# Kernel optimization log

Measured on AMD Instinct MI355X. Metric: run time of the kernel, lower is better.

Reference implementation:

```python
import jax, jax.numpy as jnp
import numpy as np

FP8_MAX = 448.0   # torch.finfo(float8_e4m3fn).max
BLK = 128         # block_size = [128, 128] for weights; [1, 128] for activations
E, H, I, T, TOPK = 8, 2048, 1408, 512, 2
FP8 = jnp.float8_e4m3fn


def fp8_round(x):
    """Round-trip through float8_e4m3fn (simulates .to(float8_e4m3fn))."""
    return jnp.clip(x, -FP8_MAX, FP8_MAX).astype(FP8).astype(jnp.float32)


def setup_inputs() -> dict:
    key = jax.random.key(0)
    ks = jax.random.split(key, 7)
    hidden_states = jax.random.normal(ks[0], (T, H), jnp.float32)
    top_k_index = jax.random.randint(ks[1], (T, TOPK), 0, E)
    top_k_weights = jax.random.uniform(ks[2], (T, TOPK), jnp.float32)
    # FP8 weight codes (stored as fp32 values exactly representable in e4m3fn)
    gate_up_proj = fp8_round(jax.random.normal(ks[3], (E, 2 * I, H), jnp.float32))
    gate_up_proj_scale_inv = jax.random.uniform(ks[4], (E, (2 * I) // BLK, H // BLK), jnp.float32, 1e-4, 1e-2)
    down_proj = fp8_round(jax.random.normal(ks[5], (E, H, I), jnp.float32))
    down_proj_scale_inv = jax.random.uniform(ks[6], (E, H // BLK, I // BLK), jnp.float32, 1e-4, 1e-2)
    return {
        "hidden_states": hidden_states,
        "top_k_index": top_k_index,
        "top_k_weights": top_k_weights,
        "gate_up_proj": gate_up_proj,
        "gate_up_proj_scale_inv": gate_up_proj_scale_inv,
        "down_proj": down_proj,
        "down_proj_scale_inv": down_proj_scale_inv,
    }


def dequant_weight(wq, s):
    # wq: [E, N, K] fp8 codes; s: [E, N//BLK, K//BLK] per-128x128-block scale_inv
    e, n, k = wq.shape
    wb = wq.reshape(e, n // BLK, BLK, k // BLK, BLK)
    return (wb * s[:, :, None, :, None]).reshape(e, n, k)


def quant_dequant_act(x):
    # dynamic per-(row, 128-block) fp8 activation quantization, then dequant
    shp = x.shape
    xb = x.reshape(shp[:-1] + (shp[-1] // BLK, BLK))
    amax = jnp.max(jnp.abs(xb), axis=-1, keepdims=True)
    scale = jnp.maximum(amax, 1e-12) / FP8_MAX
    q = fp8_round(xb / scale)
    return (q * scale).reshape(shp)


def reference(hidden_states, top_k_index, top_k_weights, gate_up_proj,
              gate_up_proj_scale_inv, down_proj, down_proj_scale_inv):
    w_gu = dequant_weight(gate_up_proj, gate_up_proj_scale_inv)  # [E, 2I, H]
    w_d = dequant_weight(down_proj, down_proj_scale_inv)         # [E, H, I]
    # activation quantization is per-token-block, so unrouted tokens are
    # unaffected; dense per-expert compute + combine-weight mask equals the
    # original gather/scatter loop exactly (unrouted contributions weight 0).
    x = quant_dequant_act(hidden_states)                         # [T, H]
    gate_up = jnp.einsum('th,enh->etn', x, w_gu)                 # [E, T, 2I]
    gate, up = jnp.split(gate_up, 2, axis=-1)
    h = jax.nn.silu(gate) * up                                   # [E, T, I]
    h = quant_dequant_act(h)
    down = jnp.einsum('eti,ehi->eth', h, w_d)                    # [E, T, H]
    # combine[t, e] = sum over top-k slots routing token t to expert e
    combine = jnp.sum(jax.nn.one_hot(top_k_index, E, dtype=top_k_weights.dtype)
                      * top_k_weights[..., None], axis=1)        # [T, E]
    out = jnp.einsum('eth,te->th', down, combine)
    return out.astype(hidden_states.dtype)
```

## Files before the change

kernel.cpp:

```cpp
#include <hip/hip_runtime.h>
#include <math.h>

#define NE 8
#define HD 2048
#define ID 1408
#define NT 512
#define FP8MAX 448.0f

typedef __attribute__((ext_vector_type(4))) float floatx4;

__device__ __forceinline__ floatx4 fzero4() {
    floatx4 z; z.x = 0.f; z.y = 0.f; z.z = 0.f; z.w = 0.f; return z;
}

#define OFF_OFFS  0
#define OFF_TOK   1024
#define OFF_WGT   8192
#define OFF_ENT   16384
#define OFF_XSG   32768
#define OFF_XG    131072
#define OFF_HS    (3*1024*1024)
#define OFF_HQ    (3*1024*1024 + 65536)
#define OFF_GU0   (5*1024*1024)
#define OFF_GU1   (17*1024*1024)

#define LDA 136

__global__ void route_kernel(const int* __restrict__ tki,
                             const float* __restrict__ tkw,
                             int* __restrict__ offs,
                             int* __restrict__ tok,
                             float* __restrict__ wgt,
                             int* __restrict__ ent) {
    __shared__ int cnt[NE];
    __shared__ int cur[NE];
    __shared__ int base[NE + 1];
    int tid = threadIdx.x;
    if (tid < NE) { cnt[tid] = 0; cur[tid] = 0; }
    __syncthreads();
    int e = tki[tid];
    atomicAdd(&cnt[e], 1);
    __syncthreads();
    if (tid == 0) {
        int s = 0;
        for (int i = 0; i < NE; i++) { base[i] = s; s += cnt[i]; }
        base[NE] = s;
    }
    __syncthreads();
    int pos = atomicAdd(&cur[e], 1);
    int j = base[e] + pos;
    tok[j] = tid >> 1;
    wgt[j] = tkw[tid];
    ent[tid] = j;
    if (tid <= NE) offs[tid] = base[tid];
}

__global__ void quant_x_kernel(const float* __restrict__ x,
                               const int* __restrict__ ent,
                               unsigned char* __restrict__ xg,
                               float* __restrict__ xsg) {
    int wid = (blockIdx.x * 256 + threadIdx.x) >> 6;
    int lane = threadIdx.x & 63;
    int t = wid >> 4;
    int b = wid & 15;
    const float2 v = *(const float2*)(x + (long)t * HD + b * 128 + lane * 2);
    float am = fmaxf(fabsf(v.x), fabsf(v.y));
    #pragma unroll
    for (int m = 32; m; m >>= 1) am = fmaxf(am, __shfl_xor(am, m));
    float scale = fmaxf(am, 1e-12f) / FP8MAX;
    int p = __builtin_amdgcn_cvt_pk_fp8_f32(v.x / scale, v.y / scale, 0, false);
    unsigned short pk = (unsigned short)(p & 0xffff);
    int e0 = ent[2 * t], e1 = ent[2 * t + 1];
    *(unsigned short*)(xg + (long)e0 * HD + b * 128 + lane * 2) = pk;
    *(unsigned short*)(xg + (long)e1 * HD + b * 128 + lane * 2) = pk;
    if (lane == 0) { xsg[e0 * 16 + b] = scale; xsg[e1 * 16 + b] = scale; }
}

__global__ void quant_h_kernel(const float* __restrict__ gu0,
                               const float* __restrict__ gu1,
                               unsigned char* __restrict__ hq,
                               float* __restrict__ hs) {
    int wid = (blockIdx.x * 256 + threadIdx.x) >> 6;
    int lane = threadIdx.x & 63;
    int j = wid / 11;
    int b = wid - j * 11;
    long base = (long)j * 2816 + b * 128 + lane * 2;
    float2 ga = *(const float2*)(gu0 + base);
    float2 gb = *(const float2*)(gu1 + base);
    float2 ua = *(const float2*)(gu0 + base + 1408);
    float2 ub = *(const float2*)(gu1 + base + 1408);
    float gx = ga.x + gb.x, gy = ga.y + gb.y;
    float ux = ua.x + ub.x, uy = ua.y + ub.y;
    float hx = (gx / (1.0f + expf(-gx))) * ux;
    float hy = (gy / (1.0f + expf(-gy))) * uy;
    float am = fmaxf(fabsf(hx), fabsf(hy));
    #pragma unroll
    for (int m = 32; m; m >>= 1) am = fmaxf(am, __shfl_xor(am, m));
    float scale = fmaxf(am, 1e-12f) / FP8MAX;
    int p = __builtin_amdgcn_cvt_pk_fp8_f32(hx / scale, hy / scale, 0, false);
    *(unsigned short*)(hq + (long)j * ID + b * 128 + lane * 2) =
        (unsigned short)(p & 0xffff);
    if (lane == 0) hs[j * 11 + b] = scale;
}

__global__ __launch_bounds__(256, 3) void gemm1_kernel(
    const unsigned char* __restrict__ xg,
    const float* __restrict__ xsg,
    const float* __restrict__ wgu,
    const float* __restrict__ sgu,
    const int* __restrict__ offs,
    float* __restrict__ gu0,
    float* __restrict__ gu1) {
    int e = blockIdx.z;
    int mt = blockIdx.y;
    int jb = blockIdx.x >> 1;
    int kh = blockIdx.x & 1;
    int o0 = offs[e], o1 = offs[e + 1];
    int ne = o1 - o0;
    int m0 = mt * 128;
    if (m0 >= ne) return;
    int rem = ne - m0;
    int j0 = o0 + m0;

    __shared__ __align__(16) unsigned char Asm[128 * LDA];
    __shared__ __align__(16) unsigned char Bsm[64 * LDA];
    __shared__ __align__(16) float sxa[128 * 20];

    int tid = threadIdx.x;
    {
        int r = tid >> 1, q = tid & 1;
        int j = j0 + r; if (j >= o1) j = o0;
        float4 s0 = *(const float4*)(xsg + j * 16 + q * 8);
        float4 s1 = *(const float4*)(xsg + j * 16 + q * 8 + 4);
        *(float4*)&sxa[r * 20 + q * 8] = s0;
        *(float4*)&sxa[r * 20 + q * 8 + 4] = s1;
    }

    int wave = tid >> 6;
    int lane = tid & 63;
    int lr = lane & 15;
    int lq = lane >> 4;

    int aseg = tid & 7;
    int arow0 = tid >> 3;
    const unsigned char* aBase0;
    const unsigned char* aBase1;
    const unsigned char* aBase2;
    const unsigned char* aBase3;
    {
        int j;
        j = j0 + arow0;       if (j >= o1) j = o0; aBase0 = xg + (long)j * HD + aseg * 16;
        j = j0 + 32 + arow0;  if (j >= o1) j = o0; aBase1 = xg + (long)j * HD + aseg * 16;
        j = j0 + 64 + arow0;  if (j >= o1) j = o0; aBase2 = xg + (long)j * HD + aseg * 16;
        j = j0 + 96 + arow0;  if (j >= o1) j = o0; aBase3 = xg + (long)j * HD + aseg * 16;
    }

    int bcol = tid & 31;
    int brow0 = tid >> 5;
    const float* bG = wgu + ((long)e * 2816 + jb * 32 + brow0) * HD + bcol * 4;
    const float* bU = wgu + ((long)e * 2816 + 1408 + jb * 32 + brow0) * HD + bcol * 4;
    const float* sgp = sgu + (e * 22 + (jb >> 2)) * 16;
    const float* sup = sgu + (e * 22 + 11 + (jb >> 2)) * 16;

    floatx4 facc[8];
    #pragma unroll
    for (int i = 0; i < 8; i++) facc[i] = fzero4();

    for (int kb = kh * 8; kb < kh * 8 + 8; kb++) {
        {
            uint4 a0 = *(const uint4*)(aBase0 + kb * 128);
            uint4 a1 = *(const uint4*)(aBase1 + kb * 128);
            uint4 a2 = *(const uint4*)(aBase2 + kb * 128);
            uint4 a3 = *(const uint4*)(aBase3 + kb * 128);
            float4 f0 = *(const float4*)(bG + kb * 128);
            float4 f1 = *(const float4*)(bG + kb * 128 + 8 * HD);
            float4 f2 = *(const float4*)(bG + kb * 128 + 16 * HD);
            float4 f3 = *(const float4*)(bG + kb * 128 + 24 * HD);
            float4 f4 = *(const float4*)(bU + kb * 128);
            float4 f5 = *(const float4*)(bU + kb * 128 + 8 * HD);
            float4 f6 = *(const float4*)(bU + kb * 128 + 16 * HD);
            float4 f7 = *(const float4*)(bU + kb * 128 + 24 * HD);
            *(uint4*)(&Asm[(arow0)      * LDA + aseg * 16]) = a0;
            *(uint4*)(&Asm[(arow0 + 32) * LDA + aseg * 16]) = a1;
            *(uint4*)(&Asm[(arow0 + 64) * LDA + aseg * 16]) = a2;
            *(uint4*)(&Asm[(arow0 + 96) * LDA + aseg * 16]) = a3;
            int p0 = __builtin_amdgcn_cvt_pk_fp8_f32(f0.x, f0.y, 0, false);
            p0 = __builtin_amdgcn_cvt_pk_fp8_f32(f0.z, f0.w, p0, true);
            int p1 = __builtin_amdgcn_cvt_pk_fp8_f32(f1.x, f1.y, 0, false);
            p1 = __builtin_amdgcn_cvt_pk_fp8_f32(f1.z, f1.w, p1, true);
            int p2 = __builtin_amdgcn_cvt_pk_fp8_f32(f2.x, f2.y, 0, false);
            p2 = __builtin_amdgcn_cvt_pk_fp8_f32(f2.z, f2.w, p2, true);
            int p3 = __builtin_amdgcn_cvt_pk_fp8_f32(f3.x, f3.y, 0, false);
            p3 = __builtin_amdgcn_cvt_pk_fp8_f32(f3.z, f3.w, p3, true);
            int p4 = __builtin_amdgcn_cvt_pk_fp8_f32(f4.x, f4.y, 0, false);
            p4 = __builtin_amdgcn_cvt_pk_fp8_f32(f4.z, f4.w, p4, true);
            int p5 = __builtin_amdgcn_cvt_pk_fp8_f32(f5.x, f5.y, 0, false);
            p5 = __builtin_amdgcn_cvt_pk_fp8_f32(f5.z, f5.w, p5, true);
            int p6 = __builtin_amdgcn_cvt_pk_fp8_f32(f6.x, f6.y, 0, false);
            p6 = __builtin_amdgcn_cvt_pk_fp8_f32(f6.z, f6.w, p6, true);
            int p7 = __builtin_amdgcn_cvt_pk_fp8_f32(f7.x, f7.y, 0, false);
            p7 = __builtin_amdgcn_cvt_pk_fp8_f32(f7.z, f7.w, p7, true);
            *(unsigned int*)(&Bsm[(brow0)      * LDA + bcol * 4]) = (unsigned int)p0;
            *(unsigned int*)(&Bsm[(brow0 + 8)  * LDA + bcol * 4]) = (unsigned int)p1;
            *(unsigned int*)(&Bsm[(brow0 + 16) * LDA + bcol * 4]) = (unsigned int)p2;
            *(unsigned int*)(&Bsm[(brow0 + 24) * LDA + bcol * 4]) = (unsigned int)p3;
            *(unsigned int*)(&Bsm[(brow0 + 32) * LDA + bcol * 4]) = (unsigned int)p4;
            *(unsigned int*)(&Bsm[(brow0 + 40) * LDA + bcol * 4]) = (unsigned int)p5;
            *(unsigned int*)(&Bsm[(brow0 + 48) * LDA + bcol * 4]) = (unsigned int)p6;
            *(unsigned int*)(&Bsm[(brow0 + 56) * LDA + bcol * 4]) = (unsigned int)p7;
        }
        __syncthreads();
        floatx4 cacc[8];
        #pragma unroll
        for (int i = 0; i < 8; i++) cacc[i] = fzero4();
        #pragma unroll
        for (int ks = 0; ks < 4; ks++) {
            long a[2], b[4];
            #pragma unroll
            for (int mi = 0; mi < 2; mi++)
                a[mi] = *(const long*)(&Asm[(wave * 32 + mi * 16 + lr) * LDA + ks * 32 + lq * 8]);
            #pragma unroll
            for (int ni = 0; ni < 4; ni++)
                b[ni] = *(const long*)(&Bsm[(ni * 16 + lr) * LDA + ks * 32 + lq * 8]);
            #pragma unroll
            for (int mi = 0; mi < 2; mi++)
                #pragma unroll
                for (int ni = 0; ni < 4; ni++)
                    cacc[mi * 4 + ni] = __builtin_amdgcn_mfma_f32_16x16x32_fp8_fp8(
                        a[mi], b[ni], cacc[mi * 4 + ni], 0, 0, 0);
        }
        float sg = sgp[kb];
        float su = sup[kb];
        #pragma unroll
        for (int mi = 0; mi < 2; mi++) {
            #pragma unroll
            for (int reg = 0; reg < 4; reg++) {
                float sx = sxa[(wave * 32 + mi * 16 + lq * 4 + reg) * 20 + kb];
                #pragma unroll
                for (int ni = 0; ni < 4; ni++) {
                    float sw = (ni < 2) ? sg : su;
                    facc[mi * 4 + ni][reg] += cacc[mi * 4 + ni][reg] * (sw * sx);
                }
            }
        }
        __syncthreads();
    }

    float* gu = kh ? gu1 : gu0;
    #pragma unroll
    for (int mi = 0; mi < 2; mi++) {
        #pragma unroll
        for (int ni = 0; ni < 4; ni++) {
            #pragma unroll
            for (int reg = 0; reg < 4; reg++) {
                int r = wave * 32 + mi * 16 + lq * 4 + reg;
                if (r < rem) {
                    long base = (long)(j0 + r) * 2816;
                    long col = (ni < 2) ? (jb * 32 + ni * 16 + lr)
                                        : (1408 + jb * 32 + (ni - 2) * 16 + lr);
                    gu[base + col] = facc[mi * 4 + ni][reg];
                }
            }
        }
    }
}

__global__ __launch_bounds__(256, 4) void gemm2_kernel(
    const unsigned char* __restrict__ hq,
    const float* __restrict__ hs,
    const float* __restrict__ wd,
    const float* __restrict__ sd,
    const int* __restrict__ offs,
    const int* __restrict__ tok,
    const float* __restrict__ wgt,
    float* __restrict__ out) {
    int e = blockIdx.z;
    int mt = blockIdx.y;
    int jb = blockIdx.x >> 1;
    int kh = blockIdx.x & 1;
    int o0 = offs[e], o1 = offs[e + 1];
    int ne = o1 - o0;
    int m0 = mt * 128;
    if (m0 >= ne) return;
    int rem = ne - m0;
    int j0 = o0 + m0;

    __shared__ __align__(16) unsigned char Asm[128 * LDA];
    __shared__ __align__(16) unsigned char Bsm[32 * LDA];
    __shared__ __align__(16) float sha[128 * 12];
    __shared__ int tokL[128];
    __shared__ float wgtL[128];

    int tid = threadIdx.x;
    if (tid < 128) {
        int j = j0 + tid;
        int valid = j < o1;
        if (!valid) j = o0;
        tokL[tid] = tok[j];
        wgtL[tid] = valid ? wgt[j] : 0.0f;
        const float* s = hs + j * 11;
        #pragma unroll
        for (int k = 0; k < 11; k++) sha[tid * 12 + k] = s[k];
    }

    int wave = tid >> 6;
    int lane = tid & 63;
    int lr = lane & 15;
    int lq = lane >> 4;

    int aseg = tid & 7;
    int arow0 = tid >> 3;
    const unsigned char* aBase0;
    const unsigned char* aBase1;
    const unsigned char* aBase2;
    const unsigned char* aBase3;
    {
        int j;
        j = j0 + arow0;       if (j >= o1) j = o0; aBase0 = hq + (long)j * ID + aseg * 16;
        j = j0 + 32 + arow0;  if (j >= o1) j = o0; aBase1 = hq + (long)j * ID + aseg * 16;
        j = j0 + 64 + arow0;  if (j >= o1) j = o0; aBase2 = hq + (long)j * ID + aseg * 16;
        j = j0 + 96 + arow0;  if (j >= o1) j = o0; aBase3 = hq + (long)j * ID + aseg * 16;
    }

    int bcol = tid & 31;
    int brow0 = tid >> 5;
    const float* bB = wd + ((long)e * HD + jb * 32 + brow0) * ID + bcol * 4;
    const float* sdp = sd + (e * 16 + (jb >> 2)) * 11;

    floatx4 facc[4];
    #pragma unroll
    for (int i = 0; i < 4; i++) facc[i] = fzero4();

    int kb0 = kh ? 6 : 0, kb1 = kh ? 11 : 6;
    for (int kb = kb0; kb < kb1; kb++) {
        {
            uint4 a0 = *(const uint4*)(aBase0 + kb * 128);
            uint4 a1 = *(const uint4*)(aBase1 + kb * 128);
            uint4 a2 = *(const uint4*)(aBase2 + kb * 128);
            uint4 a3 = *(const uint4*)(aBase3 + kb * 128);
            float4 f0 = *(const float4*)(bB + kb * 128);
            float4 f1 = *(const float4*)(bB + kb * 128 + 8 * ID);
            float4 f2 = *(const float4*)(bB + kb * 128 + 16 * ID);
            float4 f3 = *(const float4*)(bB + kb * 128 + 24 * ID);
            *(uint4*)(&Asm[(arow0)      * LDA + aseg * 16]) = a0;
            *(uint4*)(&Asm[(arow0 + 32) * LDA + aseg * 16]) = a1;
            *(uint4*)(&Asm[(arow0 + 64) * LDA + aseg * 16]) = a2;
            *(uint4*)(&Asm[(arow0 + 96) * LDA + aseg * 16]) = a3;
            int p0 = __builtin_amdgcn_cvt_pk_fp8_f32(f0.x, f0.y, 0, false);
            p0 = __builtin_amdgcn_cvt_pk_fp8_f32(f0.z, f0.w, p0, true);
            int p1 = __builtin_amdgcn_cvt_pk_fp8_f32(f1.x, f1.y, 0, false);
            p1 = __builtin_amdgcn_cvt_pk_fp8_f32(f1.z, f1.w, p1, true);
            int p2 = __builtin_amdgcn_cvt_pk_fp8_f32(f2.x, f2.y, 0, false);
            p2 = __builtin_amdgcn_cvt_pk_fp8_f32(f2.z, f2.w, p2, true);
            int p3 = __builtin_amdgcn_cvt_pk_fp8_f32(f3.x, f3.y, 0, false);
            p3 = __builtin_amdgcn_cvt_pk_fp8_f32(f3.z, f3.w, p3, true);
            *(unsigned int*)(&Bsm[(brow0)      * LDA + bcol * 4]) = (unsigned int)p0;
            *(unsigned int*)(&Bsm[(brow0 + 8)  * LDA + bcol * 4]) = (unsigned int)p1;
            *(unsigned int*)(&Bsm[(brow0 + 16) * LDA + bcol * 4]) = (unsigned int)p2;
            *(unsigned int*)(&Bsm[(brow0 + 24) * LDA + bcol * 4]) = (unsigned int)p3;
        }
        __syncthreads();
        floatx4 cacc[4];
        #pragma unroll
        for (int i = 0; i < 4; i++) cacc[i] = fzero4();
        #pragma unroll
        for (int ks = 0; ks < 4; ks++) {
            long a[2], b[2];
            #pragma unroll
            for (int mi = 0; mi < 2; mi++)
                a[mi] = *(const long*)(&Asm[(wave * 32 + mi * 16 + lr) * LDA + ks * 32 + lq * 8]);
            #pragma unroll
            for (int ni = 0; ni < 2; ni++)
                b[ni] = *(const long*)(&Bsm[(ni * 16 + lr) * LDA + ks * 32 + lq * 8]);
            #pragma unroll
            for (int mi = 0; mi < 2; mi++)
                #pragma unroll
                for (int ni = 0; ni < 2; ni++)
                    cacc[mi * 2 + ni] = __builtin_amdgcn_mfma_f32_16x16x32_fp8_fp8(
                        a[mi], b[ni], cacc[mi * 2 + ni], 0, 0, 0);
        }
        float sw = sdp[kb];
        #pragma unroll
        for (int mi = 0; mi < 2; mi++) {
            #pragma unroll
            for (int reg = 0; reg < 4; reg++) {
                float sh = sha[(wave * 32 + mi * 16 + lq * 4 + reg) * 12 + kb];
                #pragma unroll
                for (int ni = 0; ni < 2; ni++)
                    facc[mi * 2 + ni][reg] += cacc[mi * 2 + ni][reg] * (sw * sh);
            }
        }
        __syncthreads();
    }

    #pragma unroll
    for (int mi = 0; mi < 2; mi++) {
        #pragma unroll
        for (int ni = 0; ni < 2; ni++) {
            #pragma unroll
            for (int reg = 0; reg < 4; reg++) {
                int r = wave * 32 + mi * 16 + lq * 4 + reg;
                if (r < rem) {
                    float v = facc[mi * 2 + ni][reg] * wgtL[r];
                    atomicAdd(out + (long)tokL[r] * HD + jb * 32 + ni * 16 + lr, v);
                }
            }
        }
    }
}

extern "C" void kernel_launch(void* const* d_in, const int* in_sizes, int n_in,
                              void* d_out, int out_size, void* d_ws, size_t ws_size,
                              hipStream_t stream) {
    (void)in_sizes; (void)n_in; (void)out_size; (void)ws_size;
    const float* x   = (const float*)d_in[0];
    const int*   tki = (const int*)d_in[1];
    const float* tkw = (const float*)d_in[2];
    const float* wgu = (const float*)d_in[3];
    const float* sgu = (const float*)d_in[4];
    const float* wd  = (const float*)d_in[5];
    const float* sd  = (const float*)d_in[6];
    float* out = (float*)d_out;
    char* ws = (char*)d_ws;

    int*   offs = (int*)(ws + OFF_OFFS);
    int*   tok  = (int*)(ws + OFF_TOK);
    float* wgt  = (float*)(ws + OFF_WGT);
    int*   ent  = (int*)(ws + OFF_ENT);
    float* xsg  = (float*)(ws + OFF_XSG);
    unsigned char* xg = (unsigned char*)(ws + OFF_XG);
    float* hs   = (float*)(ws + OFF_HS);
    unsigned char* hq = (unsigned char*)(ws + OFF_HQ);
    float* gu0  = (float*)(ws + OFF_GU0);
    float* gu1  = (float*)(ws + OFF_GU1);

    hipMemsetAsync(d_out, 0, (size_t)NT * HD * sizeof(float), stream);
    route_kernel<<<1, 1024, 0, stream>>>(tki, tkw, offs, tok, wgt, ent);
    quant_x_kernel<<<2048, 256, 0, stream>>>(x, ent, xg, xsg);
    gemm1_kernel<<<dim3(88, 8, NE), 256, 0, stream>>>(xg, xsg, wgu, sgu, offs, gu0, gu1);
    quant_h_kernel<<<2816, 256, 0, stream>>>(gu0, gu1, hq, hs);
    gemm2_kernel<<<dim3(128, 8, NE), 256, 0, stream>>>(hq, hs, wd, sd, offs, tok, wgt, out);
}
```

Baseline: 363.1 us.

## Loop m-tiles inside GEMM blocks and replace atomic scatter with combine kernel

Both expert GEMM kernels drop the grid dimension over 128-row tiles. Each block now loops over all of its expert's row tiles, which removes the many blocks that used to exit immediately. gemm2 no longer does weighted atomicAdd into the zeroed output. It writes per-slot partial results (one buffer per K-half, reusing the gate/up workspace), and a new combine kernel reads each token's two slots, weights them and writes the output, so the memset goes away. The trade-off is that experts with more than one row tile now process those tiles serially, and there is an extra kernel launch. gemm1's launch bound also rises from 3 to 4 blocks per CU.

Result: slower. 381.3 us (+5.0%).

```diff
diff --git a/kernel.cpp b/kernel.cpp
--- a/kernel.cpp
+++ b/kernel.cpp
@@ -103,7 +103,7 @@
     if (lane == 0) hs[j * 11 + b] = scale;
 }
 
-__global__ __launch_bounds__(256, 3) void gemm1_kernel(
+__global__ __launch_bounds__(256, 4) void gemm1_kernel(
     const unsigned char* __restrict__ xg,
     const float* __restrict__ xsg,
     const float* __restrict__ wgu,
@@ -112,48 +112,21 @@
     float* __restrict__ gu0,
     float* __restrict__ gu1) {
     int e = blockIdx.z;
-    int mt = blockIdx.y;
     int jb = blockIdx.x >> 1;
     int kh = blockIdx.x & 1;
     int o0 = offs[e], o1 = offs[e + 1];
     int ne = o1 - o0;
-    int m0 = mt * 128;
-    if (m0 >= ne) return;
-    int rem = ne - m0;
-    int j0 = o0 + m0;
+    if (ne <= 0) return;
 
     __shared__ __align__(16) unsigned char Asm[128 * LDA];
     __shared__ __align__(16) unsigned char Bsm[64 * LDA];
     __shared__ __align__(16) float sxa[128 * 20];
 
     int tid = threadIdx.x;
-    {
-        int r = tid >> 1, q = tid & 1;
-        int j = j0 + r; if (j >= o1) j = o0;
-        float4 s0 = *(const float4*)(xsg + j * 16 + q * 8);
-        float4 s1 = *(const float4*)(xsg + j * 16 + q * 8 + 4);
-        *(float4*)&sxa[r * 20 + q * 8] = s0;
-        *(float4*)&sxa[r * 20 + q * 8 + 4] = s1;
-    }
-
     int wave = tid >> 6;
     int lane = tid & 63;
     int lr = lane & 15;
     int lq = lane >> 4;
-
-    int aseg = tid & 7;
-    int arow0 = tid >> 3;
-    const unsigned char* aBase0;
-    const unsigned char* aBase1;
-    const unsigned char* aBase2;
-    const unsigned char* aBase3;
-    {
-        int j;
-        j = j0 + arow0;       if (j >= o1) j = o0; aBase0 = xg + (long)j * HD + aseg * 16;
-        j = j0 + 32 + arow0;  if (j >= o1) j = o0; aBase1 = xg + (long)j * HD + aseg * 16;
-        j = j0 + 64 + arow0;  if (j >= o1) j = o0; aBase2 = xg + (long)j * HD + aseg * 16;
-        j = j0 + 96 + arow0;  if (j >= o1) j = o0; aBase3 = xg + (long)j * HD + aseg * 16;
-    }
 
     int bcol = tid & 31;
     int brow0 = tid >> 5;
@@ -162,103 +135,133 @@
     const float* sgp = sgu + (e * 22 + (jb >> 2)) * 16;
     const float* sup = sgu + (e * 22 + 11 + (jb >> 2)) * 16;
 
-    floatx4 facc[8];
-    #pragma unroll
-    for (int i = 0; i < 8; i++) facc[i] = fzero4();
-
-    for (int kb = kh * 8; kb < kh * 8 + 8; kb++) {
+    int aseg = tid & 7;
+    int arow0 = tid >> 3;
+    int kbS = kh * 8, kbE = kbS + 8;
+
+    for (int m0 = 0; m0 < ne; m0 += 128) {
+        int rem = ne - m0;
+        int j0 = o0 + m0;
+
         {
-            uint4 a0 = *(const uint4*)(aBase0 + kb * 128);
-            uint4 a1 = *(const uint4*)(aBase1 + kb * 128);
-            uint4 a2 = *(const uint4*)(aBase2 + kb * 128);
-            uint4 a3 = *(const uint4*)(aBase3 + kb * 128);
-            float4 f0 = *(const float4*)(bG + kb * 128);
-            float4 f1 = *(const float4*)(bG + kb * 128 + 8 * HD);
-            float4 f2 = *(const float4*)(bG + kb * 128 + 16 * HD);
-            float4 f3 = *(const float4*)(bG + kb * 128 + 24 * HD);
-            float4 f4 = *(const float4*)(bU + kb * 128);
-            float4 f5 = *(const float4*)(bU + kb * 128 + 8 * HD);
-            float4 f6 = *(const float4*)(bU + kb * 128 + 16 * HD);
-            float4 f7 = *(const float4*)(bU + kb * 128 + 24 * HD);
-            *(uint4*)(&Asm[(arow0)      * LDA + aseg * 16]) = a0;
-            *(uint4*)(&Asm[(arow0 + 32) * LDA + aseg * 16]) = a1;
-            *(uint4*)(&Asm[(arow0 + 64) * LDA + aseg * 16]) = a2;
-            *(uint4*)(&Asm[(arow0 + 96) * LDA + aseg * 16]) = a3;
-            int p0 = __builtin_amdgcn_cvt_pk_fp8_f32(f0.x, f0.y, 0, false);
-            p0 = __builtin_amdgcn_cvt_pk_fp8_f32(f0.z, f0.w, p0, true);
-            int p1 = __builtin_amdgcn_cvt_pk_fp8_f32(f1.x, f1.y, 0, false);
-            p1 = __builtin_amdgcn_cvt_pk_fp8_f32(f1.z, f1.w, p1, true);
-            int p2 = __builtin_amdgcn_cvt_pk_fp8_f32(f2.x, f2.y, 0, false);
-            p2 = __builtin_amdgcn_cvt_pk_fp8_f32(f2.z, f2.w, p2, true);
-            int p3 = __builtin_amdgcn_cvt_pk_fp8_f32(f3.x, f3.y, 0, false);
-            p3 = __builtin_amdgcn_cvt_pk_fp8_f32(f3.z, f3.w, p3, true);
-            int p4 = __builtin_amdgcn_cvt_pk_fp8_f32(f4.x, f4.y, 0, false);
-            p4 = __builtin_amdgcn_cvt_pk_fp8_f32(f4.z, f4.w, p4, true);
-            int p5 = __builtin_amdgcn_cvt_pk_fp8_f32(f5.x, f5.y, 0, false);
-            p5 = __builtin_amdgcn_cvt_pk_fp8_f32(f5.z, f5.w, p5, true);
-            int p6 = __builtin_amdgcn_cvt_pk_fp8_f32(f6.x, f6.y, 0, false);
-            p6 = __builtin_amdgcn_cvt_pk_fp8_f32(f6.z, f6.w, p6, true);
-            int p7 = __builtin_amdgcn_cvt_pk_fp8_f32(f7.x, f7.y, 0, false);
-            p7 = __builtin_amdgcn_cvt_pk_fp8_f32(f7.z, f7.w, p7, true);
-            *(unsigned int*)(&Bsm[(brow0)      * LDA + bcol * 4]) = (unsigned int)p0;
-            *(unsigned int*)(&Bsm[(brow0 + 8)  * LDA + bcol * 4]) = (unsigned int)p1;
-            *(unsigned int*)(&Bsm[(brow0 + 16) * LDA + bcol * 4]) = (unsigned int)p2;
-            *(unsigned int*)(&Bsm[(brow0 + 24) * LDA + bcol * 4]) = (unsigned int)p3;
-            *(unsigned int*)(&Bsm[(brow0 + 32) * LDA + bcol * 4]) = (unsigned int)p4;
-            *(unsigned int*)(&Bsm[(brow0 + 40) * LDA + bcol * 4]) = (unsigned int)p5;
-            *(unsigned int*)(&Bsm[(brow0 + 48) * LDA + bcol * 4]) = (unsigned int)p6;
-            *(unsigned int*)(&Bsm[(brow0 + 56) * LDA + bcol * 4]) = (unsigned int)p7;
-        }
-        __syncthreads();
-        floatx4 cacc[8];
+            int r = tid >> 1, q = tid & 1;
+            int j = j0 + r; if (j >= o1) j = o0;
+            float4 s0 = *(const float4*)(xsg + j * 16 + q * 8);
+            float4 s1 = *(const float4*)(xsg + j * 16 + q * 8 + 4);
+            *(float4*)&sxa[r * 20 + q * 8] = s0;
+            *(float4*)&sxa[r * 20 + q * 8 + 4] = s1;
+        }
+
+        const unsigned char* aBase0;
+        const unsigned char* aBase1;
+        const unsigned char* aBase2;
+        const unsigned char* aBase3;
+        {
+            int j;
+            j = j0 + arow0;       if (j >= o1) j = o0; aBase0 = xg + (long)j * HD + aseg * 16;
+            j = j0 + 32 + arow0;  if (j >= o1) j = o0; aBase1 = xg + (long)j * HD + aseg * 16;
+            j = j0 + 64 + arow0;  if (j >= o1) j = o0; aBase2 = xg + (long)j * HD + aseg * 16;
+            j = j0 + 96 + arow0;  if (j >= o1) j = o0; aBase3 = xg + (long)j * HD + aseg * 16;
+        }
+
+        floatx4 facc[8];
         #pragma unroll
-        for (int i = 0; i < 8; i++) cacc[i] = fzero4();
-        #pragma unroll
-        for (int ks = 0; ks < 4; ks++) {
-            long a[2], b[4];
-            #pragma unroll
-            for (int mi = 0; mi < 2; mi++)
-                a[mi] = *(const long*)(&Asm[(wave * 32 + mi * 16 + lr) * LDA + ks * 32 + lq * 8]);
-            #pragma unroll
-            for (int ni = 0; ni < 4; ni++)
-                b[ni] = *(const long*)(&Bsm[(ni * 16 + lr) * LDA + ks * 32 + lq * 8]);
-            #pragma unroll
-            for (int mi = 0; mi < 2; mi++)
+        for (int i = 0; i < 8; i++) facc[i] = fzero4();
+
+        for (int kb = kbS; kb < kbE; kb++) {
+            {
+                uint4 a0 = *(const uint4*)(aBase0 + kb * 128);
+                uint4 a1 = *(const uint4*)(aBase1 + kb * 128);
+                uint4 a2 = *(const uint4*)(aBase2 + kb * 128);
+                uint4 a3 = *(const uint4*)(aBase3 + kb * 128);
+                float4 f0 = *(const float4*)(bG + kb * 128);
+                float4 f1 = *(const float4*)(bG + kb * 128 + 8 * HD);
+                float4 f2 = *(const float4*)(bG + kb * 128 + 16 * HD);
+                float4 f3 = *(const float4*)(bG + kb * 128 + 24 * HD);
+                float4 f4 = *(const float4*)(bU + kb * 128);
+                float4 f5 = *(const float4*)(bU + kb * 128 + 8 * HD);
+                float4 f6 = *(const float4*)(bU + kb * 128 + 16 * HD);
+                float4 f7 = *(const float4*)(bU + kb * 128 + 24 * HD);
+                *(uint4*)(&Asm[(arow0)      * LDA + aseg * 16]) = a0;
+                *(uint4*)(&Asm[(arow0 + 32) * LDA + aseg * 16]) = a1;
+                *(uint4*)(&Asm[(arow0 + 64) * LDA + aseg * 16]) = a2;
+                *(uint4*)(&Asm[(arow0 + 96) * LDA + aseg * 16]) = a3;
+                int p0 = __builtin_amdgcn_cvt_pk_fp8_f32(f0.x, f0.y, 0, false);
+                p0 = __builtin_amdgcn_cvt_pk_fp8_f32(f0.z, f0.w, p0, true);
+                int p1 = __builtin_amdgcn_cvt_pk_fp8_f32(f1.x, f1.y, 0, false);
+                p1 = __builtin_amdgcn_cvt_pk_fp8_f32(f1.z, f1.w, p1, true);
+                int p2 = __builtin_amdgcn_cvt_pk_fp8_f32(f2.x, f2.y, 0, false);
+                p2 = __builtin_amdgcn_cvt_pk_fp8_f32(f2.z, f2.w, p2, true);
+                int p3 = __builtin_amdgcn_cvt_pk_fp8_f32(f3.x, f3.y, 0, false);
+                p3 = __builtin_amdgcn_cvt_pk_fp8_f32(f3.z, f3.w, p3, true);
+                int p4 = __builtin_amdgcn_cvt_pk_fp8_f32(f4.x, f4.y, 0, false);
+                p4 = __builtin_amdgcn_cvt_pk_fp8_f32(f4.z, f4.w, p4, true);
+                int p5 = __builtin_amdgcn_cvt_pk_fp8_f32(f5.x, f5.y, 0, false);
+                p5 = __builtin_amdgcn_cvt_pk_fp8_f32(f5.z, f5.w, p5, true);
+                int p6 = __builtin_amdgcn_cvt_pk_fp8_f32(f6.x, f6.y, 0, false);
+                p6 = __builtin_amdgcn_cvt_pk_fp8_f32(f6.z, f6.w, p6, true);
+                int p7 = __builtin_amdgcn_cvt_pk_fp8_f32(f7.x, f7.y, 0, false);
+                p7 = __builtin_amdgcn_cvt_pk_fp8_f32(f7.z, f7.w, p7, true);
+                *(unsigned int*)(&Bsm[(brow0)      * LDA + bcol * 4]) = (unsigned int)p0;
+                *(unsigned int*)(&Bsm[(brow0 + 8)  * LDA + bcol * 4]) = (unsigned int)p1;
+                *(unsigned int*)(&Bsm[(brow0 + 16) * LDA + bcol * 4]) = (unsigned int)p2;
+                *(unsigned int*)(&Bsm[(brow0 + 24) * LDA + bcol * 4]) = (unsigned int)p3;
+                *(unsigned int*)(&Bsm[(brow0 + 32) * LDA + bcol * 4]) = (unsigned int)p4;
+                *(unsigned int*)(&Bsm[(brow0 + 40) * LDA + bcol * 4]) = (unsigned int)p5;
+                *(unsigned int*)(&Bsm[(brow0 + 48) * LDA + bcol * 4]) = (unsigned int)p6;
+                *(unsigned int*)(&Bsm[(brow0 + 56) * LDA + bcol * 4]) = (unsigned int)p7;
+            }
+            __syncthreads();
+            floatx4 cacc[8];
+            #pragma unroll
+            for (int i = 0; i < 8; i++) cacc[i] = fzero4();
+            #pragma unroll
+            for (int ks = 0; ks < 4; ks++) {
+                long a[2], b[4];
+                #pragma unroll
+                for (int mi = 0; mi < 2; mi++)
+                    a[mi] = *(const long*)(&Asm[(wave * 32 + mi * 16 + lr) * LDA + ks * 32 + lq * 8]);
                 #pragma unroll
                 for (int ni = 0; ni < 4; ni++)
-                    cacc[mi * 4 + ni] = __builtin_amdgcn_mfma_f32_16x16x32_fp8_fp8(
-                        a[mi], b[ni], cacc[mi * 4 + ni], 0, 0, 0);
-        }
-        float sg = sgp[kb];
-        float su = sup[kb];
+                    b[ni] = *(const long*)(&Bsm[(ni * 16 + lr) * LDA + ks * 32 + lq * 8]);
+                #pragma unroll
+                for (int mi = 0; mi < 2; mi++)
+                    #pragma unroll
+                    for (int ni = 0; ni < 4; ni++)
+                        cacc[mi * 4 + ni] = __builtin_amdgcn_mfma_f32_16x16x32_fp8_fp8(
+                            a[mi], b[ni], cacc[mi * 4 + ni], 0, 0, 0);
+            }
+            float sg = sgp[kb];
+            float su = sup[kb];
+            #pragma unroll
+            for (int mi = 0; mi < 2; mi++) {
+                #pragma unroll
+                for (int reg = 0; reg < 4; reg++) {
+                    float sx = sxa[(wave * 32 + mi * 16 + lq * 4 + reg) * 20 + kb];
+                    #pragma unroll
+                    for (int ni = 0; ni < 4; ni++) {
+                        float sw = (ni < 2) ? sg : su;
+                        facc[mi * 4 + ni][reg] += cacc[mi * 4 + ni][reg] * (sw * sx);
+                    }
+                }
+            }
+            __syncthreads();
+        }
+
+        float* gu = kh ? gu1 : gu0;
         #pragma unroll
         for (int mi = 0; mi < 2; mi++) {
             #pragma unroll
-            for (int reg = 0; reg < 4; reg++) {
-                float sx = sxa[(wave * 32 + mi * 16 + lq * 4 + reg) * 20 + kb];
-                #pragma unroll
-                for (int ni = 0; ni < 4; ni++) {
-                    float sw = (ni < 2) ? sg : su;
-                    facc[mi * 4 + ni][reg] += cacc[mi * 4 + ni][reg] * (sw * sx);
-                }
-            }
-        }
-        __syncthreads();
-    }
-
-    float* gu = kh ? gu1 : gu0;
-    #pragma unroll
-    for (int mi = 0; mi < 2; mi++) {
-        #pragma unroll
-        for (int ni = 0; ni < 4; ni++) {
-            #pragma unroll
-            for (int reg = 0; reg < 4; reg++) {
-                int r = wave * 32 + mi * 16 + lq * 4 + reg;
-                if (r < rem) {
-                    long base = (long)(j0 + r) * 2816;
-                    long col = (ni < 2) ? (jb * 32 + ni * 16 + lr)
-                                        : (1408 + jb * 32 + (ni - 2) * 16 + lr);
-                    gu[base + col] = facc[mi * 4 + ni][reg];
+            for (int ni = 0; ni < 4; ni++) {
+                #pragma unroll
+                for (int reg = 0; reg < 4; reg++) {
+                    int r = wave * 32 + mi * 16 + lq * 4 + reg;
+                    if (r < rem) {
+                        long base = (long)(j0 + r) * 2816;
+                        long col = (ni < 2) ? (jb * 32 + ni * 16 + lr)
+                                            : (1408 + jb * 32 + (ni - 2) * 16 + lr);
+                        gu[base + col] = facc[mi * 4 + ni][reg];
+                    }
                 }
             }
         }
@@ -271,38 +274,20 @@
     const float* __restrict__ wd,
     const float* __restrict__ sd,
     const int* __restrict__ offs,
-    const int* __restrict__ tok,
-    const float* __restrict__ wgt,
-    float* __restrict__ out) {
+    float* __restrict__ d0,
+    float* __restrict__ d1) {
     int e = blockIdx.z;
-    int mt = blockIdx.y;
     int jb = blockIdx.x >> 1;
     int kh = blockIdx.x & 1;
     int o0 = offs[e], o1 = offs[e + 1];
     int ne = o1 - o0;
-    int m0 = mt * 128;
-    if (m0 >= ne) return;
-    int rem = ne - m0;
-    int j0 = o0 + m0;
+    if (ne <= 0) return;
 
     __shared__ __align__(16) unsigned char Asm[128 * LDA];
     __shared__ __align__(16) unsigned char Bsm[32 * LDA];
     __shared__ __align__(16) float sha[128 * 12];
-    __shared__ int tokL[128];
-    __shared__ float wgtL[128];
 
     int tid = threadIdx.x;
-    if (tid < 128) {
-        int j = j0 + tid;
-        int valid = j < o1;
-        if (!valid) j = o0;
-        tokL[tid] = tok[j];
-        wgtL[tid] = valid ? wgt[j] : 0.0f;
-        const float* s = hs + j * 11;
-        #pragma unroll
-        for (int k = 0; k < 11; k++) sha[tid * 12 + k] = s[k];
-    }
-
     int wave = tid >> 6;
     int lane = tid & 63;
     int lr = lane & 15;
@@ -310,103 +295,143 @@
 
     int aseg = tid & 7;
     int arow0 = tid >> 3;
-    const unsigned char* aBase0;
-    const unsigned char* aBase1;
-    const unsigned char* aBase2;
-    const unsigned char* aBase3;
-    {
-        int j;
-        j = j0 + arow0;       if (j >= o1) j = o0; aBase0 = hq + (long)j * ID + aseg * 16;
-        j = j0 + 32 + arow0;  if (j >= o1) j = o0; aBase1 = hq + (long)j * ID + aseg * 16;
-        j = j0 + 64 + arow0;  if (j >= o1) j = o0; aBase2 = hq + (long)j * ID + aseg * 16;
-        j = j0 + 96 + arow0;  if (j >= o1) j = o0; aBase3 = hq + (long)j * ID + aseg * 16;
-    }
 
     int bcol = tid & 31;
     int brow0 = tid >> 5;
     const float* bB = wd + ((long)e * HD + jb * 32 + brow0) * ID + bcol * 4;
     const float* sdp = sd + (e * 16 + (jb >> 2)) * 11;
 
-    floatx4 facc[4];
-    #pragma unroll
-    for (int i = 0; i < 4; i++) facc[i] = fzero4();
-
     int kb0 = kh ? 6 : 0, kb1 = kh ? 11 : 6;
-    for (int kb = kb0; kb < kb1; kb++) {
+    float* dp = kh ? d1 : d0;
+
+    for (int m0 = 0; m0 < ne; m0 += 128) {
+        int rem = ne - m0;
+        int j0 = o0 + m0;
+
+        if (tid < 128) {
+            int j = j0 + tid;
+            if (j >= o1) j = o0;
+            const float* s = hs + j * 11;
+            #pragma unroll
+            for (int k = 0; k < 11; k++) sha[tid * 12 + k] = s[k];
+        }
+
+        const unsigned char* aBase0;
+        const unsigned char* aBase1;
+        const unsigned char* aBase2;
+        const unsigned char* aBase3;
         {
-            uint4 a0 = *(const uint4*)(aBase0 + kb * 128);
-            uint4 a1 = *(const uint4*)(aBase1 + kb * 128);
-            uint4 a2 = *(const uint4*)(aBase2 + kb * 128);
-            uint4 a3 = *(const uint4*)(aBase3 + kb * 128);
-            float4 f0 = *(const float4*)(bB + kb * 128);
-            float4 f1 = *(const float4*)(bB + kb * 128 + 8 * ID);
-            float4 f2 = *(const float4*)(bB + kb * 128 + 16 * ID);
-            float4 f3 = *(const float4*)(bB + kb * 128 + 24 * ID);
-            *(uint4*)(&Asm[(arow0)      * LDA + aseg * 16]) = a0;
-            *(uint4*)(&Asm[(arow0 + 32) * LDA + aseg * 16]) = a1;
-            *(uint4*)(&Asm[(arow0 + 64) * LDA + aseg * 16]) = a2;
-            *(uint4*)(&Asm[(arow0 + 96) * LDA + aseg * 16]) = a3;
-            int p0 = __builtin_amdgcn_cvt_pk_fp8_f32(f0.x, f0.y, 0, false);
-            p0 = __builtin_amdgcn_cvt_pk_fp8_f32(f0.z, f0.w, p0, true);
-            int p1 = __builtin_amdgcn_cvt_pk_fp8_f32(f1.x, f1.y, 0, false);
-            p1 = __builtin_amdgcn_cvt_pk_fp8_f32(f1.z, f1.w, p1, true);
-            int p2 = __builtin_amdgcn_cvt_pk_fp8_f32(f2.x, f2.y, 0, false);
-            p2 = __builtin_amdgcn_cvt_pk_fp8_f32(f2.z, f2.w, p2, true);
-            int p3 = __builtin_amdgcn_cvt_pk_fp8_f32(f3.x, f3.y, 0, false);
-            p3 = __builtin_amdgcn_cvt_pk_fp8_f32(f3.z, f3.w, p3, true);
-            *(unsigned int*)(&Bsm[(brow0)      * LDA + bcol * 4]) = (unsigned int)p0;
-            *(unsigned int*)(&Bsm[(brow0 + 8)  * LDA + bcol * 4]) = (unsigned int)p1;
-            *(unsigned int*)(&Bsm[(brow0 + 16) * LDA + bcol * 4]) = (unsigned int)p2;
-            *(unsigned int*)(&Bsm[(brow0 + 24) * LDA + bcol * 4]) = (unsigned int)p3;
-        }
-        __syncthreads();
-        floatx4 cacc[4];
+            int j;
+            j = j0 + arow0;       if (j >= o1) j = o0; aBase0 = hq + (long)j * ID + aseg * 16;
+            j = j0 + 32 + arow0;  if (j >= o1) j = o0; aBase1 = hq + (long)j * ID + aseg * 16;
+            j = j0 + 64 + arow0;  if (j >= o1) j = o0; aBase2 = hq + (long)j * ID + aseg * 16;
+            j = j0 + 96 + arow0;  if (j >= o1) j = o0; aBase3 = hq + (long)j * ID + aseg * 16;
+        }
+
+        floatx4 facc[4];
         #pragma unroll
-        for (int i = 0; i < 4; i++) cacc[i] = fzero4();
-        #pragma unroll
-        for (int ks = 0; ks < 4; ks++) {
-            long a[2], b[2];
-            #pragma unroll
-            for (int mi = 0; mi < 2; mi++)
-                a[mi] = *(const long*)(&Asm[(wave * 32 + mi * 16 + lr) * LDA + ks * 32 + lq * 8]);
-            #pragma unroll
-            for (int ni = 0; ni < 2; ni++)
-                b[ni] = *(const long*)(&Bsm[(ni * 16 + lr) * LDA + ks * 32 + lq * 8]);
-            #pragma unroll
-            for (int mi = 0; mi < 2; mi++)
+        for (int i = 0; i < 4; i++) facc[i] = fzero4();
+
+        for (int kb = kb0; kb < kb1; kb++) {
+            {
+                uint4 a0 = *(const uint4*)(aBase0 + kb * 128);
+                uint4 a1 = *(const uint4*)(aBase1 + kb * 128);
+                uint4 a2 = *(const uint4*)(aBase2 + kb * 128);
+                uint4 a3 = *(const uint4*)(aBase3 + kb * 128);
+                float4 f0 = *(const float4*)(bB + kb * 128);
+                float4 f1 = *(const float4*)(bB + kb * 128 + 8 * ID);
+                float4 f2 = *(const float4*)(bB + kb * 128 + 16 * ID);
+                float4 f3 = *(const float4*)(bB + kb * 128 + 24 * ID);
+                *(uint4*)(&Asm[(arow0)      * LDA + aseg * 16]) = a0;
+                *(uint4*)(&Asm[(arow0 + 32) * LDA + aseg * 16]) = a1;
+                *(uint4*)(&Asm[(arow0 + 64) * LDA + aseg * 16]) = a2;
+                *(uint4*)(&Asm[(arow0 + 96) * LDA + aseg * 16]) = a3;
+                int p0 = __builtin_amdgcn_cvt_pk_fp8_f32(f0.x, f0.y, 0, false);
+                p0 = __builtin_amdgcn_cvt_pk_fp8_f32(f0.z, f0.w, p0, true);
+                int p1 = __builtin_amdgcn_cvt_pk_fp8_f32(f1.x, f1.y, 0, false);
+                p1 = __builtin_amdgcn_cvt_pk_fp8_f32(f1.z, f1.w, p1, true);
+                int p2 = __builtin_amdgcn_cvt_pk_fp8_f32(f2.x, f2.y, 0, false);
+                p2 = __builtin_amdgcn_cvt_pk_fp8_f32(f2.z, f2.w, p2, true);
+                int p3 = __builtin_amdgcn_cvt_pk_fp8_f32(f3.x, f3.y, 0, false);
+                p3 = __builtin_amdgcn_cvt_pk_fp8_f32(f3.z, f3.w, p3, true);
+                *(unsigned int*)(&Bsm[(brow0)      * LDA + bcol * 4]) = (unsigned int)p0;
+                *(unsigned int*)(&Bsm[(brow0 + 8)  * LDA + bcol * 4]) = (unsigned int)p1;
+                *(unsigned int*)(&Bsm[(brow0 + 16) * LDA + bcol * 4]) = (unsigned int)p2;
+                *(unsigned int*)(&Bsm[(brow0 + 24) * LDA + bcol * 4]) = (unsigned int)p3;
+            }
+            __syncthreads();
+            floatx4 cacc[4];
+            #pragma unroll
+            for (int i = 0; i < 4; i++) cacc[i] = fzero4();
+            #pragma unroll
+            for (int ks = 0; ks < 4; ks++) {
+                long a[2], b[2];
+                #pragma unroll
+                for (int mi = 0; mi < 2; mi++)
+                    a[mi] = *(const long*)(&Asm[(wave * 32 + mi * 16 + lr) * LDA + ks * 32 + lq * 8]);
                 #pragma unroll
                 for (int ni = 0; ni < 2; ni++)
-                    cacc[mi * 2 + ni] = __builtin_amdgcn_mfma_f32_16x16x32_fp8_fp8(
-                        a[mi], b[ni], cacc[mi * 2 + ni], 0, 0, 0);
-        }
-        float sw = sdp[kb];
+                    b[ni] = *(const long*)(&Bsm[(ni * 16 + lr) * LDA + ks * 32 + lq * 8]);
+                #pragma unroll
+                for (int mi = 0; mi < 2; mi++)
+                    #pragma unroll
+                    for (int ni = 0; ni < 2; ni++)
+                        cacc[mi * 2 + ni] = __builtin_amdgcn_mfma_f32_16x16x32_fp8_fp8(
+                            a[mi], b[ni], cacc[mi * 2 + ni], 0, 0, 0);
+            }
+            float sw = sdp[kb];
+            #pragma unroll
+            for (int mi = 0; mi < 2; mi++) {
+                #pragma unroll
+                for (int reg = 0; reg < 4; reg++) {
+                    float sh = sha[(wave * 32 + mi * 16 + lq * 4 + reg) * 12 + kb];
+                    #pragma unroll
+                    for (int ni = 0; ni < 2; ni++)
+                        facc[mi * 2 + ni][reg] += cacc[mi * 2 + ni][reg] * (sw * sh);
+                }
+            }
+            __syncthreads();
+        }
+
         #pragma unroll
         for (int mi = 0; mi < 2; mi++) {
             #pragma unroll
-            for (int reg = 0; reg < 4; reg++) {
-                float sh = sha[(wave * 32 + mi * 16 + lq * 4 + reg) * 12 + kb];
-                #pragma unroll
-                for (int ni = 0; ni < 2; ni++)
-                    facc[mi * 2 + ni][reg] += cacc[mi * 2 + ni][reg] * (sw * sh);
-            }
-        }
-        __syncthreads();
+            for (int ni = 0; ni < 2; ni++) {
+                #pragma unroll
+                for (int reg = 0; reg < 4; reg++) {
+                    int r = wave * 32 + mi * 16 + lq * 4 + reg;
+                    if (r < rem) {
+                        dp[(long)(j0 + r) * HD + jb * 32 + ni * 16 + lr] =
+                            facc[mi * 2 + ni][reg];
+                    }
+                }
+            }
+        }
     }
-
-    #pragma unroll
-    for (int mi = 0; mi < 2; mi++) {
-        #pragma unroll
-        for (int ni = 0; ni < 2; ni++) {
-            #pragma unroll
-            for (int reg = 0; reg < 4; reg++) {
-                int r = wave * 32 + mi * 16 + lq * 4 + reg;
-                if (r < rem) {
-                    float v = facc[mi * 2 + ni][reg] * wgtL[r];
-                    atomicAdd(out + (long)tokL[r] * HD + jb * 32 + ni * 16 + lr, v);
-                }
-            }
-        }
-    }
+}
+
+__global__ void combine_kernel(const float* __restrict__ d0,
+                               const float* __restrict__ d1,
+                               const int* __restrict__ ent,
+                               const float* __restrict__ tkw,
+                               float* __restrict__ out) {
+    int gid = blockIdx.x * 256 + threadIdx.x;
+    int t = gid >> 9;
+    int c4 = gid & 511;
+    int j0 = ent[2 * t], j1 = ent[2 * t + 1];
+    float w0 = tkw[2 * t], w1 = tkw[2 * t + 1];
+    long b0 = (long)j0 * HD + c4 * 4;
+    long b1 = (long)j1 * HD + c4 * 4;
+    float4 a0 = *(const float4*)(d0 + b0);
+    float4 a1 = *(const float4*)(d1 + b0);
+    float4 a2 = *(const float4*)(d0 + b1);
+    float4 a3 = *(const float4*)(d1 + b1);
+    float4 r;
+    r.x = w0 * (a0.x + a1.x) + w1 * (a2.x + a3.x);
+    r.y = w0 * (a0.y + a1.y) + w1 * (a2.y + a3.y);
+    r.z = w0 * (a0.z + a1.z) + w1 * (a2.z + a3.z);
+    r.w = w0 * (a0.w + a1.w) + w1 * (a2.w + a3.w);
+    *(float4*)(out + (long)t * HD + c4 * 4) = r;
 }
 
 extern "C" void kernel_launch(void* const* d_in, const int* in_sizes, int n_in,
@@ -433,11 +458,13 @@
     unsigned char* hq = (unsigned char*)(ws + OFF_HQ);
     float* gu0  = (float*)(ws + OFF_GU0);
     float* gu1  = (float*)(ws + OFF_GU1);
-
-    hipMemsetAsync(d_out, 0, (size_t)NT * HD * sizeof(float), stream);
+    float* dp0  = (float*)(ws + OFF_GU0);
+    float* dp1  = (float*)(ws + OFF_GU1);
+
     route_kernel<<<1, 1024, 0, stream>>>(tki, tkw, offs, tok, wgt, ent);
     quant_x_kernel<<<2048, 256, 0, stream>>>(x, ent, xg, xsg);
-    gemm1_kernel<<<dim3(88, 8, NE), 256, 0, stream>>>(xg, xsg, wgu, sgu, offs, gu0, gu1);
+    gemm1_kernel<<<dim3(88, 1, NE), 256, 0, stream>>>(xg, xsg, wgu, sgu, offs, gu0, gu1);
     quant_h_kernel<<<2816, 256, 0, stream>>>(gu0, gu1, hq, hs);
-    gemm2_kernel<<<dim3(128, 8, NE), 256, 0, stream>>>(hq, hs, wd, sd, offs, tok, wgt, out);
-}
+    gemm2_kernel<<<dim3(128, 1, NE), 256, 0, stream>>>(hq, hs, wd, sd, offs, dp0, dp1);
+    combine_kernel<<<1024, 256, 0, stream>>>(dp0, dp1, ent, tkw, out);
+}
```
